# Kernel optimization log

Hardware: AMD Instinct MI355X
Metric: run time of the kernel (lower is better)

The kernel has to match this reference:

```python
import jax, jax.numpy as jnp
import numpy as np

B, S, H, D = 4, 1024, 16, 64
DM = H * D  # 1024
SCALE = float(np.sqrt(D))


def setup_inputs() -> dict:
    key = jax.random.key(0)
    ks = jax.random.split(key, 7)
    mk = lambda k, shp: jax.random.normal(k, shp, dtype=jnp.float32)
    return {
        "query": mk(ks[0], (B, S, DM)),
        "key": mk(ks[1], (B, S, DM)),
        "value": mk(ks[2], (B, S, DM)),
        "Wq": mk(ks[3], (DM, DM)) * 0.02,
        "Wk": mk(ks[4], (DM, DM)) * 0.02,
        "Wv": mk(ks[5], (DM, DM)) * 0.02,
        "Wo": mk(ks[6], (DM, DM)) * 0.02,
    }


def reference(query, key, value, Wq, Wk, Wv, Wo):
    b, s, _ = query.shape
    # nn.Linear(x) = x @ W.T ; reshape to (b, h, s, d)
    Q = (query @ Wq.T).reshape(b, s, H, D).transpose(0, 2, 1, 3)
    K = (key @ Wk.T).reshape(b, s, H, D).transpose(0, 2, 1, 3)
    V = (value @ Wv.T).reshape(b, s, H, D).transpose(0, 2, 1, 3)
    scores = jnp.einsum("bhqd,bhkd->bhqk", Q, K) / SCALE
    attn = jax.nn.softmax(scores, axis=-1)  # dropout p=0 -> identity
    ctx = jnp.einsum("bhqk,bhkd->bhqd", attn, V)
    ctx = ctx.transpose(0, 2, 1, 3).reshape(b, s, DM)
    out = ctx @ Wo.T
    return out, attn
```

## Files before the change

kernel.cpp:

```cpp
#include <hip/hip_runtime.h>
#include <hip/hip_bf16.h>
#include <stdint.h>


#define DEV static __device__ __forceinline__

typedef __bf16 bf16x8 __attribute__((ext_vector_type(8)));
typedef float f32x4 __attribute__((ext_vector_type(4)));
typedef unsigned short u16x8 __attribute__((ext_vector_type(8)));

static constexpr int B = 4, S = 1024, H = 16, D = 64, DM = 1024;
static constexpr int M = B * S;

DEV uint16_t f2bf_bits(float f) {
    __hip_bfloat16 h = __float2bfloat16(f);
    return __builtin_bit_cast(uint16_t, h);
}
DEV uint64_t pack4(float4 v) {
    return (uint64_t)f2bf_bits(v.x) | ((uint64_t)f2bf_bits(v.y) << 16) |
           ((uint64_t)f2bf_bits(v.z) << 32) | ((uint64_t)f2bf_bits(v.w) << 48);
}
DEV bf16x8 ldfrag(const uint16_t* p) {
    u16x8 t = *(const u16x8*)p;
    return __builtin_bit_cast(bf16x8, t);
}

#define GLOAD16(g, l)                                                  \
    __builtin_amdgcn_global_load_lds(                                  \
        (const __attribute__((address_space(1))) void*)(g),            \
        (__attribute__((address_space(3))) void*)(l), 16, 0, 0)

#define MFMA16(a, b, c) __builtin_amdgcn_mfma_f32_16x16x32_bf16(a, b, c, 0, 0, 0)

__global__ __launch_bounds__(256) void cvt_w4(const float* __restrict__ w0,
                                              const float* __restrict__ w1,
                                              const float* __restrict__ w2,
                                              const float* __restrict__ w3,
                                              uint16_t* __restrict__ dst) {
    const float* srcs[4] = {w0, w1, w2, w3};
    const float* src = srcs[blockIdx.y];
    uint16_t* d = dst + (size_t)blockIdx.y * DM * DM;
    int i = (blockIdx.x * 256 + threadIdx.x) * 8;
    float4 a = *(const float4*)(src + i);
    float4 b = *(const float4*)(src + i + 4);
    *(uint64_t*)(d + i) = pack4(a);
    *(uint64_t*)(d + i + 4) = pack4(b);
}

__global__ __launch_bounds__(256) void gemm_qkv(const float* __restrict__ qa,
                                                const float* __restrict__ ka,
                                                const float* __restrict__ va,
                                                const uint16_t* __restrict__ Wb,
                                                uint16_t* __restrict__ Qb,
                                                uint16_t* __restrict__ Kb,
                                                uint16_t* __restrict__ Vt) {
    constexpr int BK = 32;
    __shared__ uint16_t Ah[128 * BK];
    __shared__ uint16_t Bh[128 * BK];
    const int tid = threadIdx.x;
    const int lane = tid & 63, wid = tid >> 6;
    const int lr = lane & 15, lg = lane >> 4;
    const int m0 = blockIdx.x * 128, n0 = blockIdx.y * 128;
    const int z = blockIdx.z;
    const int wr = (wid >> 1) * 64, wc = (wid & 1) * 64;

    const float* A = z == 0 ? qa : (z == 1 ? ka : va);
    const uint16_t* W = Wb + (size_t)z * DM * DM;
    uint16_t* Cp = z == 0 ? Qb : (z == 1 ? Kb : Vt);

    const int arow = tid >> 1, acs = (tid & 1) * 16;
    const int brow = wid * 16 + (lane >> 2), bcol = (lane & 3) * 8;

    f32x4 acc[4][4] = {};

    for (int kb = 0; kb < DM / BK; ++kb) {
        const float* ap = A + (size_t)(m0 + arow) * DM + kb * BK + acs;
        float4 v0 = *(const float4*)(ap + 0);
        float4 v1 = *(const float4*)(ap + 4);
        float4 v2 = *(const float4*)(ap + 8);
        float4 v3 = *(const float4*)(ap + 12);
#pragma unroll
        for (int c = 0; c < 2; ++c) {
            int row = c * 64 + brow;
            GLOAD16(W + (size_t)(n0 + row) * DM + kb * BK + bcol, Bh + row * BK + bcol);
        }
        uint16_t* aw = Ah + arow * BK + acs;
        *(uint64_t*)(aw + 0) = pack4(v0);
        *(uint64_t*)(aw + 4) = pack4(v1);
        *(uint64_t*)(aw + 8) = pack4(v2);
        *(uint64_t*)(aw + 12) = pack4(v3);
        __syncthreads();

        bf16x8 af[4], bw[4];
#pragma unroll
        for (int i = 0; i < 4; ++i) af[i] = ldfrag(&Ah[(wr + i * 16 + lr) * BK + lg * 8]);
#pragma unroll
        for (int i = 0; i < 4; ++i) bw[i] = ldfrag(&Bh[(wc + i * 16 + lr) * BK + lg * 8]);
#pragma unroll
        for (int mi = 0; mi < 4; ++mi)
#pragma unroll
            for (int ni = 0; ni < 4; ++ni)
                acc[mi][ni] = MFMA16(af[mi], bw[ni], acc[mi][ni]);
        __syncthreads();
    }

#pragma unroll
    for (int mi = 0; mi < 4; ++mi)
#pragma unroll
        for (int ni = 0; ni < 4; ++ni)
#pragma unroll
            for (int r = 0; r < 4; ++r) {
                int gm = m0 + wr + mi * 16 + lg * 4 + r;
                int gn = n0 + wc + ni * 16 + lr;
                uint16_t v = f2bf_bits(acc[mi][ni][r]);
                int b = gm >> 10, s = gm & 1023, h = gn >> 6, d = gn & 63;
                if (z != 2)
                    Cp[((size_t)(b * H + h) * S + s) * D + d] = v;
                else
                    Cp[((size_t)(b * H + h) * D + d) * S + s] = v;
            }
}

__global__ __launch_bounds__(256) void gemm_o(const uint16_t* __restrict__ ctx,
                                              const uint16_t* __restrict__ Wo,
                                              float* __restrict__ out) {
    constexpr int BK = 32;
    __shared__ uint16_t Ah[128 * BK];
    __shared__ uint16_t Bh[128 * BK];
    const int tid = threadIdx.x;
    const int lane = tid & 63, wid = tid >> 6;
    const int lr = lane & 15, lg = lane >> 4;
    const int m0 = blockIdx.x * 128, n0 = blockIdx.y * 128;
    const int wr = (wid >> 1) * 64, wc = (wid & 1) * 64;
    const int srow = wid * 16 + (lane >> 2), scol = (lane & 3) * 8;

    f32x4 acc[4][4] = {};

    for (int kb = 0; kb < DM / BK; ++kb) {
#pragma unroll
        for (int c = 0; c < 2; ++c) {
            int row = c * 64 + srow;
            GLOAD16(ctx + (size_t)(m0 + row) * DM + kb * BK + scol, Ah + row * BK + scol);
            GLOAD16(Wo + (size_t)(n0 + row) * DM + kb * BK + scol, Bh + row * BK + scol);
        }
        __syncthreads();

        bf16x8 af[4], bw[4];
#pragma unroll
        for (int i = 0; i < 4; ++i) af[i] = ldfrag(&Ah[(wr + i * 16 + lr) * BK + lg * 8]);
#pragma unroll
        for (int i = 0; i < 4; ++i) bw[i] = ldfrag(&Bh[(wc + i * 16 + lr) * BK + lg * 8]);
#pragma unroll
        for (int mi = 0; mi < 4; ++mi)
#pragma unroll
            for (int ni = 0; ni < 4; ++ni)
                acc[mi][ni] = MFMA16(af[mi], bw[ni], acc[mi][ni]);
        __syncthreads();
    }

#pragma unroll
    for (int mi = 0; mi < 4; ++mi)
#pragma unroll
        for (int ni = 0; ni < 4; ++ni)
#pragma unroll
            for (int r = 0; r < 4; ++r) {
                int gm = m0 + wr + mi * 16 + lg * 4 + r;
                int gn = n0 + wc + ni * 16 + lr;
                out[(size_t)gm * DM + gn] = acc[mi][ni][r];
            }
}

__global__ __launch_bounds__(256) void attn_fused(const uint16_t* __restrict__ Qb,
                                                  const uint16_t* __restrict__ Kb,
                                                  const uint16_t* __restrict__ Vt,
                                                  float* __restrict__ attn,
                                                  uint16_t* __restrict__ ctx) {
    __shared__ uint16_t plds[4][16][40];
    const int tid = threadIdx.x, lane = tid & 63, wid = tid >> 6;
    const int lr = lane & 15, lg = lane >> 4;
    const int wg = blockIdx.x;
    const int xcd = wg & 7, rr_ = wg >> 3;
    const int qt = rr_ & 15, bh = xcd + 8 * (rr_ >> 4);
    const int q0 = qt * 64 + wid * 16;

    const uint16_t* Qp = Qb + ((size_t)bh * S + q0) * D;
    const bf16x8 aq0 = ldfrag(Qp + lr * D + lg * 8);
    const bf16x8 aq1 = ldfrag(Qp + lr * D + 32 + lg * 8);

    const uint16_t* Kbase = Kb + (size_t)bh * S * D;
    constexpr float CEXP = 0.125f * 1.44269504088896340736f;

    float lsum[4] = {0.f, 0.f, 0.f, 0.f};
    for (int kc = 0; kc < S / 32; ++kc) {
        const uint16_t* Kp = Kbase + (size_t)kc * 32 * D;
        bf16x8 k00 = ldfrag(Kp + lr * D + lg * 8);
        bf16x8 k01 = ldfrag(Kp + lr * D + 32 + lg * 8);
        bf16x8 k10 = ldfrag(Kp + (16 + lr) * D + lg * 8);
        bf16x8 k11 = ldfrag(Kp + (16 + lr) * D + 32 + lg * 8);
        f32x4 s0 = {}, s1 = {};
        s0 = MFMA16(aq0, k00, s0);
        s0 = MFMA16(aq1, k01, s0);
        s1 = MFMA16(aq0, k10, s1);
        s1 = MFMA16(aq1, k11, s1);
#pragma unroll
        for (int r = 0; r < 4; ++r)
            lsum[r] += exp2f(s0[r] * CEXP) + exp2f(s1[r] * CEXP);
    }
#pragma unroll
    for (int r = 0; r < 4; ++r) {
        float v = lsum[r];
        v += __shfl_xor(v, 1);
        v += __shfl_xor(v, 2);
        v += __shfl_xor(v, 4);
        v += __shfl_xor(v, 8);
        lsum[r] = 1.0f / v;
    }

    f32x4 cacc[4] = {};
    float* attn_base = attn + (size_t)bh * S * S + (size_t)q0 * S;
    const uint16_t* Vbase = Vt + (size_t)bh * D * S;
    uint16_t(*pw)[40] = plds[wid];

    for (int kc = 0; kc < S / 32; ++kc) {
        const uint16_t* Kp = Kbase + (size_t)kc * 32 * D;
        bf16x8 k00 = ldfrag(Kp + lr * D + lg * 8);
        bf16x8 k01 = ldfrag(Kp + lr * D + 32 + lg * 8);
        bf16x8 k10 = ldfrag(Kp + (16 + lr) * D + lg * 8);
        bf16x8 k11 = ldfrag(Kp + (16 + lr) * D + 32 + lg * 8);
        bf16x8 bv[4];
#pragma unroll
        for (int dt = 0; dt < 4; ++dt)
            bv[dt] = ldfrag(Vbase + (size_t)(dt * 16 + lr) * S + kc * 32 + lg * 8);
        f32x4 s0 = {}, s1 = {};
        s0 = MFMA16(aq0, k00, s0);
        s0 = MFMA16(aq1, k01, s0);
        s1 = MFMA16(aq0, k10, s1);
        s1 = MFMA16(aq1, k11, s1);
#pragma unroll
        for (int r = 0; r < 4; ++r) {
            float p0 = exp2f(s0[r] * CEXP) * lsum[r];
            float p1 = exp2f(s1[r] * CEXP) * lsum[r];
            attn_base[(size_t)(lg * 4 + r) * S + kc * 32 + lr] = p0;
            attn_base[(size_t)(lg * 4 + r) * S + kc * 32 + 16 + lr] = p1;
            pw[lg * 4 + r][lr] = f2bf_bits(p0);
            pw[lg * 4 + r][16 + lr] = f2bf_bits(p1);
        }
        asm volatile("s_waitcnt lgkmcnt(0)" ::: "memory");
        bf16x8 pa = ldfrag(&pw[lr][lg * 8]);
#pragma unroll
        for (int dt = 0; dt < 4; ++dt)
            cacc[dt] = MFMA16(pa, bv[dt], cacc[dt]);
    }

    const int b = bh >> 4, h = bh & 15;
#pragma unroll
    for (int dt = 0; dt < 4; ++dt)
#pragma unroll
        for (int r = 0; r < 4; ++r) {
            int q = q0 + lg * 4 + r;
            int d = dt * 16 + lr;
            ctx[((size_t)b * S + q) * DM + h * D + d] = f2bf_bits(cacc[dt][r]);
        }
}

extern "C" void kernel_launch(void* const* d_in, const int* in_sizes, int n_in,
                              void* d_out, int out_size, void* d_ws, size_t ws_size,
                              hipStream_t stream) {
    const float* q = (const float*)d_in[0];
    const float* k = (const float*)d_in[1];
    const float* v = (const float*)d_in[2];
    const float* Wq = (const float*)d_in[3];
    const float* Wk = (const float*)d_in[4];
    const float* Wv = (const float*)d_in[5];
    const float* Wo = (const float*)d_in[6];

    float* out = (float*)d_out;
    float* attn = out + (size_t)B * S * DM;

    const size_t NQ = (size_t)B * H * S * D;
    uint16_t* Qb = (uint16_t*)d_ws;
    uint16_t* Kb = Qb + NQ;
    uint16_t* Vt = Kb + NQ;
    uint16_t* ctx = Vt + NQ;
    uint16_t* Wb = ctx + NQ;

    cvt_w4<<<dim3(512, 4), 256, 0, stream>>>(Wq, Wk, Wv, Wo, Wb);
    gemm_qkv<<<dim3(M / 128, DM / 128, 3), 256, 0, stream>>>(q, k, v, Wb, Qb, Kb, Vt);
    attn_fused<<<dim3(16 * 64), 256, 0, stream>>>(Qb, Kb, Vt, attn, ctx);
    gemm_o<<<dim3(M / 128, DM / 128), 256, 0, stream>>>(ctx, Wb + (size_t)3 * DM * DM, out);
}
```

Measured before the change: 561.9 us.

## Stage K/V in LDS with swizzle, coalesce attn stores, widen GEMM K tiles

The attention kernel now double-buffers K and V tiles in swizzled LDS through async global-to-LDS loads. Probabilities are staged in LDS as fp32 so the attn matrix is written with coalesced float4 stores. Both GEMMs move to BK=64, and the V projection transposes through LDS so Vt is written with vector stores. When the workspace is large enough, the activations are pre-converted to bf16 in a single conversion kernel so the QKV GEMM loads them asynchronously. The trade is extra LDS use and block-wide barriers in the attention loop.

```diff
diff --git a/kernel.cpp b/kernel.cpp
--- a/kernel.cpp
+++ b/kernel.cpp
@@ -9,8 +9,8 @@
 typedef float f32x4 __attribute__((ext_vector_type(4)));
 typedef unsigned short u16x8 __attribute__((ext_vector_type(8)));
 
-static constexpr int B = 4, S = 1024, H = 16, D = 64, DM = 1024;
-static constexpr int M = B * S;
+static constexpr int B = 4, S = 1024, H = 16, D = 64, DM = 1024, M = 4096;
+static constexpr size_t NQ = (size_t)M * DM;
 
 DEV uint16_t f2bf_bits(float f) {
     __hip_bfloat16 h = __float2bfloat16(f);
@@ -19,6 +19,10 @@
 DEV uint64_t pack4(float4 v) {
     return (uint64_t)f2bf_bits(v.x) | ((uint64_t)f2bf_bits(v.y) << 16) |
            ((uint64_t)f2bf_bits(v.z) << 32) | ((uint64_t)f2bf_bits(v.w) << 48);
+}
+DEV uint64_t pack4f(const f32x4& v) {
+    return (uint64_t)f2bf_bits(v[0]) | ((uint64_t)f2bf_bits(v[1]) << 16) |
+           ((uint64_t)f2bf_bits(v[2]) << 32) | ((uint64_t)f2bf_bits(v[3]) << 48);
 }
 DEV bf16x8 ldfrag(const uint16_t* p) {
     u16x8 t = *(const u16x8*)p;
@@ -31,6 +35,27 @@
         (__attribute__((address_space(3))) void*)(l), 16, 0, 0)
 
 #define MFMA16(a, b, c) __builtin_amdgcn_mfma_f32_16x16x32_bf16(a, b, c, 0, 0, 0)
+
+__global__ __launch_bounds__(256) void cvt_all(const float* __restrict__ q,
+                                               const float* __restrict__ k,
+                                               const float* __restrict__ v,
+                                               const float* __restrict__ wq,
+                                               const float* __restrict__ wk,
+                                               const float* __restrict__ wv,
+                                               const float* __restrict__ wo,
+                                               uint16_t* __restrict__ dst) {
+    const int y = blockIdx.y;
+    const float* srcs[7] = {q, k, v, wq, wk, wv, wo};
+    const float* src = srcs[y];
+    const size_t base = y < 3 ? (size_t)y * NQ : 3 * NQ + (size_t)(y - 3) * (DM * DM);
+    const size_t n = y < 3 ? NQ : (size_t)DM * DM;
+    size_t i = ((size_t)blockIdx.x * 256 + threadIdx.x) * 8;
+    if (i >= n) return;
+    float4 a = *(const float4*)(src + i);
+    float4 b2 = *(const float4*)(src + i + 4);
+    *(uint64_t*)(dst + base + i) = pack4(a);
+    *(uint64_t*)(dst + base + i + 4) = pack4(b2);
+}
 
 __global__ __launch_bounds__(256) void cvt_w4(const float* __restrict__ w0,
                                               const float* __restrict__ w1,
@@ -42,119 +67,149 @@
     uint16_t* d = dst + (size_t)blockIdx.y * DM * DM;
     int i = (blockIdx.x * 256 + threadIdx.x) * 8;
     float4 a = *(const float4*)(src + i);
-    float4 b = *(const float4*)(src + i + 4);
+    float4 b2 = *(const float4*)(src + i + 4);
     *(uint64_t*)(d + i) = pack4(a);
-    *(uint64_t*)(d + i + 4) = pack4(b);
-}
-
+    *(uint64_t*)(d + i + 4) = pack4(b2);
+}
+
+template <int AF32>
 __global__ __launch_bounds__(256) void gemm_qkv(const float* __restrict__ qa,
                                                 const float* __restrict__ ka,
                                                 const float* __restrict__ va,
+                                                const uint16_t* __restrict__ xb,
                                                 const uint16_t* __restrict__ Wb,
                                                 uint16_t* __restrict__ Qb,
                                                 uint16_t* __restrict__ Kb,
                                                 uint16_t* __restrict__ Vt) {
-    constexpr int BK = 32;
-    __shared__ uint16_t Ah[128 * BK];
-    __shared__ uint16_t Bh[128 * BK];
-    const int tid = threadIdx.x;
-    const int lane = tid & 63, wid = tid >> 6;
+    constexpr int BK = 64, ALD = AF32 ? 72 : 64;
+    __shared__ __align__(16) uint16_t smem[17408];
+    uint16_t* Ah = smem;
+    uint16_t* Bh = smem + (AF32 ? 9216 : 8192);
+    const int tid = threadIdx.x, lane = tid & 63, wid = tid >> 6;
     const int lr = lane & 15, lg = lane >> 4;
-    const int m0 = blockIdx.x * 128, n0 = blockIdx.y * 128;
-    const int z = blockIdx.z;
+    const int m0 = blockIdx.x * 128, n0 = blockIdx.y * 128, z = blockIdx.z;
     const int wr = (wid >> 1) * 64, wc = (wid & 1) * 64;
 
-    const float* A = z == 0 ? qa : (z == 1 ? ka : va);
-    const uint16_t* W = Wb + (size_t)z * DM * DM;
-    uint16_t* Cp = z == 0 ? Qb : (z == 1 ? Kb : Vt);
-
-    const int arow = tid >> 1, acs = (tid & 1) * 16;
-    const int brow = wid * 16 + (lane >> 2), bcol = (lane & 3) * 8;
+    const float* Af = z == 0 ? qa : (z == 1 ? ka : va);
+    const uint16_t* Ab = xb + (size_t)z * NQ;
+    const uint16_t* W = Wb + (size_t)z * (DM * DM);
 
     f32x4 acc[4][4] = {};
 
     for (int kb = 0; kb < DM / BK; ++kb) {
-        const float* ap = A + (size_t)(m0 + arow) * DM + kb * BK + acs;
-        float4 v0 = *(const float4*)(ap + 0);
-        float4 v1 = *(const float4*)(ap + 4);
-        float4 v2 = *(const float4*)(ap + 8);
-        float4 v3 = *(const float4*)(ap + 12);
-#pragma unroll
-        for (int c = 0; c < 2; ++c) {
-            int row = c * 64 + brow;
-            GLOAD16(W + (size_t)(n0 + row) * DM + kb * BK + bcol, Bh + row * BK + bcol);
-        }
-        uint16_t* aw = Ah + arow * BK + acs;
-        *(uint64_t*)(aw + 0) = pack4(v0);
-        *(uint64_t*)(aw + 4) = pack4(v1);
-        *(uint64_t*)(aw + 8) = pack4(v2);
-        *(uint64_t*)(aw + 12) = pack4(v3);
-        __syncthreads();
-
-        bf16x8 af[4], bw[4];
-#pragma unroll
-        for (int i = 0; i < 4; ++i) af[i] = ldfrag(&Ah[(wr + i * 16 + lr) * BK + lg * 8]);
-#pragma unroll
-        for (int i = 0; i < 4; ++i) bw[i] = ldfrag(&Bh[(wc + i * 16 + lr) * BK + lg * 8]);
+        if constexpr (AF32) {
+#pragma unroll
+            for (int i = 0; i < 8; ++i) {
+                int f = tid + i * 256;
+                int row = f >> 4, c4 = (f & 15) * 4;
+                float4 vv = *(const float4*)(Af + (size_t)(m0 + row) * DM + kb * BK + c4);
+                *(uint64_t*)&Ah[row * ALD + c4] = pack4(vv);
+            }
+        } else {
+#pragma unroll
+            for (int p = 0; p < 4; ++p) {
+                int row = p * 32 + (tid >> 3), ce = (tid & 7) * 8;
+                GLOAD16(Ab + (size_t)(m0 + row) * DM + kb * BK + ce, Ah + row * 64 + ce);
+            }
+        }
+#pragma unroll
+        for (int p = 0; p < 4; ++p) {
+            int row = p * 32 + (tid >> 3), ce = (tid & 7) * 8;
+            GLOAD16(W + (size_t)(n0 + row) * DM + kb * BK + ce, Bh + row * 64 + ce);
+        }
+        __syncthreads();
+
+        bf16x8 af[4][2], bw[4][2];
+#pragma unroll
+        for (int i = 0; i < 4; ++i)
+#pragma unroll
+            for (int ks = 0; ks < 2; ++ks) {
+                af[i][ks] = ldfrag(&Ah[(wr + i * 16 + lr) * ALD + ks * 32 + lg * 8]);
+                bw[i][ks] = ldfrag(&Bh[(wc + i * 16 + lr) * 64 + ks * 32 + lg * 8]);
+            }
+#pragma unroll
+        for (int ks = 0; ks < 2; ++ks)
+#pragma unroll
+            for (int mi = 0; mi < 4; ++mi)
+#pragma unroll
+                for (int ni = 0; ni < 4; ++ni)
+                    acc[mi][ni] = MFMA16(af[mi][ks], bw[ni][ks], acc[mi][ni]);
+        __syncthreads();
+    }
+
+    if (z != 2) {
+        uint16_t* Cp = z == 0 ? Qb : Kb;
 #pragma unroll
         for (int mi = 0; mi < 4; ++mi)
 #pragma unroll
             for (int ni = 0; ni < 4; ++ni)
-                acc[mi][ni] = MFMA16(af[mi], bw[ni], acc[mi][ni]);
-        __syncthreads();
-    }
-
-#pragma unroll
-    for (int mi = 0; mi < 4; ++mi)
-#pragma unroll
-        for (int ni = 0; ni < 4; ++ni)
-#pragma unroll
-            for (int r = 0; r < 4; ++r) {
-                int gm = m0 + wr + mi * 16 + lg * 4 + r;
-                int gn = n0 + wc + ni * 16 + lr;
-                uint16_t v = f2bf_bits(acc[mi][ni][r]);
-                int b = gm >> 10, s = gm & 1023, h = gn >> 6, d = gn & 63;
-                if (z != 2)
-                    Cp[((size_t)(b * H + h) * S + s) * D + d] = v;
-                else
-                    Cp[((size_t)(b * H + h) * D + d) * S + s] = v;
-            }
+#pragma unroll
+                for (int r = 0; r < 4; ++r) {
+                    int gm = m0 + wr + mi * 16 + lg * 4 + r;
+                    int gn = n0 + wc + ni * 16 + lr;
+                    int b = gm >> 10, s = gm & 1023, h = gn >> 6, d = gn & 63;
+                    Cp[((size_t)(b * H + h) * S + s) * D + d] = f2bf_bits(acc[mi][ni][r]);
+                }
+    } else {
+        uint16_t* T = smem;
+#pragma unroll
+        for (int mi = 0; mi < 4; ++mi)
+#pragma unroll
+            for (int ni = 0; ni < 4; ++ni) {
+                int row = wc + ni * 16 + lr;
+                int colb = wr + mi * 16 + lg * 4;
+                *(uint64_t*)&T[row * 136 + colb] = pack4f(acc[mi][ni]);
+            }
+        __syncthreads();
+        const int b = m0 >> 10, s0b = m0 & 1023;
+#pragma unroll
+        for (int p = 0; p < 8; ++p) {
+            int row = p * 16 + (tid >> 4), sl = tid & 15;
+            int h = (n0 + row) >> 6, d = (n0 + row) & 63;
+            u16x8 val = *(u16x8*)&T[row * 136 + sl * 8];
+            *(u16x8*)&Vt[((size_t)(b * H + h) * D + d) * S + s0b + sl * 8] = val;
+        }
+    }
 }
 
 __global__ __launch_bounds__(256) void gemm_o(const uint16_t* __restrict__ ctx,
                                               const uint16_t* __restrict__ Wo,
                                               float* __restrict__ out) {
-    constexpr int BK = 32;
-    __shared__ uint16_t Ah[128 * BK];
-    __shared__ uint16_t Bh[128 * BK];
-    const int tid = threadIdx.x;
-    const int lane = tid & 63, wid = tid >> 6;
+    constexpr int BK = 64;
+    __shared__ __align__(16) uint16_t smem[16384];
+    uint16_t* Ah = smem;
+    uint16_t* Bh = smem + 8192;
+    const int tid = threadIdx.x, lane = tid & 63, wid = tid >> 6;
     const int lr = lane & 15, lg = lane >> 4;
     const int m0 = blockIdx.x * 128, n0 = blockIdx.y * 128;
     const int wr = (wid >> 1) * 64, wc = (wid & 1) * 64;
-    const int srow = wid * 16 + (lane >> 2), scol = (lane & 3) * 8;
 
     f32x4 acc[4][4] = {};
 
     for (int kb = 0; kb < DM / BK; ++kb) {
 #pragma unroll
-        for (int c = 0; c < 2; ++c) {
-            int row = c * 64 + srow;
-            GLOAD16(ctx + (size_t)(m0 + row) * DM + kb * BK + scol, Ah + row * BK + scol);
-            GLOAD16(Wo + (size_t)(n0 + row) * DM + kb * BK + scol, Bh + row * BK + scol);
-        }
-        __syncthreads();
-
-        bf16x8 af[4], bw[4];
-#pragma unroll
-        for (int i = 0; i < 4; ++i) af[i] = ldfrag(&Ah[(wr + i * 16 + lr) * BK + lg * 8]);
-#pragma unroll
-        for (int i = 0; i < 4; ++i) bw[i] = ldfrag(&Bh[(wc + i * 16 + lr) * BK + lg * 8]);
-#pragma unroll
-        for (int mi = 0; mi < 4; ++mi)
-#pragma unroll
-            for (int ni = 0; ni < 4; ++ni)
-                acc[mi][ni] = MFMA16(af[mi], bw[ni], acc[mi][ni]);
+        for (int p = 0; p < 4; ++p) {
+            int row = p * 32 + (tid >> 3), ce = (tid & 7) * 8;
+            GLOAD16(ctx + (size_t)(m0 + row) * DM + kb * BK + ce, Ah + row * 64 + ce);
+            GLOAD16(Wo + (size_t)(n0 + row) * DM + kb * BK + ce, Bh + row * 64 + ce);
+        }
+        __syncthreads();
+
+        bf16x8 af[4][2], bw[4][2];
+#pragma unroll
+        for (int i = 0; i < 4; ++i)
+#pragma unroll
+            for (int ks = 0; ks < 2; ++ks) {
+                af[i][ks] = ldfrag(&Ah[(wr + i * 16 + lr) * 64 + ks * 32 + lg * 8]);
+                bw[i][ks] = ldfrag(&Bh[(wc + i * 16 + lr) * 64 + ks * 32 + lg * 8]);
+            }
+#pragma unroll
+        for (int ks = 0; ks < 2; ++ks)
+#pragma unroll
+            for (int mi = 0; mi < 4; ++mi)
+#pragma unroll
+                for (int ni = 0; ni < 4; ++ni)
+                    acc[mi][ni] = MFMA16(af[mi][ks], bw[ni][ks], acc[mi][ni]);
         __syncthreads();
     }
 
@@ -175,7 +230,9 @@
                                                   const uint16_t* __restrict__ Vt,
                                                   float* __restrict__ attn,
                                                   uint16_t* __restrict__ ctx) {
-    __shared__ uint16_t plds[4][16][40];
+    __shared__ __align__(16) uint16_t Kl[2][2048];
+    __shared__ __align__(16) uint16_t Vl[2][2048];
+    __shared__ __align__(16) float pf[4][16 * 36];
     const int tid = threadIdx.x, lane = tid & 63, wid = tid >> 6;
     const int lr = lane & 15, lg = lane >> 4;
     const int wg = blockIdx.x;
@@ -188,15 +245,25 @@
     const bf16x8 aq1 = ldfrag(Qp + lr * D + 32 + lg * 8);
 
     const uint16_t* Kbase = Kb + (size_t)bh * S * D;
+    const uint16_t* Vbase = Vt + (size_t)bh * D * S;
     constexpr float CEXP = 0.125f * 1.44269504088896340736f;
 
+    const int krow = tid >> 3, kslot = (tid & 7) ^ ((tid >> 3) & 7);
+    const int vrow = tid >> 2, vslot = (tid & 3) ^ ((tid >> 3) & 3);
+
+#define STAGE_K(buf, kc) GLOAD16(Kbase + (size_t)((kc)*32 + krow) * D + kslot * 8, &Kl[buf][tid * 8])
+#define STAGE_V(buf, kc) GLOAD16(Vbase + (size_t)vrow * S + (kc)*32 + vslot * 8, &Vl[buf][tid * 8])
+#define KFRAG(buf, t, h) ldfrag(&Kl[buf][((t)*16 + lr) * 64 + ((((h)*4 + lg) ^ (lr & 7)) * 8)])
+#define VFRAG(buf, dt) ldfrag(&Vl[buf][((dt)*16 + lr) * 32 + ((lg ^ ((lr >> 1) & 3)) * 8)])
+
     float lsum[4] = {0.f, 0.f, 0.f, 0.f};
+    STAGE_K(0, 0);
+    __syncthreads();
     for (int kc = 0; kc < S / 32; ++kc) {
-        const uint16_t* Kp = Kbase + (size_t)kc * 32 * D;
-        bf16x8 k00 = ldfrag(Kp + lr * D + lg * 8);
-        bf16x8 k01 = ldfrag(Kp + lr * D + 32 + lg * 8);
-        bf16x8 k10 = ldfrag(Kp + (16 + lr) * D + lg * 8);
-        bf16x8 k11 = ldfrag(Kp + (16 + lr) * D + 32 + lg * 8);
+        const int buf = kc & 1;
+        if (kc < S / 32 - 1) STAGE_K(buf ^ 1, kc + 1);
+        bf16x8 k00 = KFRAG(buf, 0, 0), k01 = KFRAG(buf, 0, 1);
+        bf16x8 k10 = KFRAG(buf, 1, 0), k11 = KFRAG(buf, 1, 1);
         f32x4 s0 = {}, s1 = {};
         s0 = MFMA16(aq0, k00, s0);
         s0 = MFMA16(aq1, k01, s0);
@@ -205,6 +272,7 @@
 #pragma unroll
         for (int r = 0; r < 4; ++r)
             lsum[r] += exp2f(s0[r] * CEXP) + exp2f(s1[r] * CEXP);
+        __syncthreads();
     }
 #pragma unroll
     for (int r = 0; r < 4; ++r) {
@@ -218,19 +286,19 @@
 
     f32x4 cacc[4] = {};
     float* attn_base = attn + (size_t)bh * S * S + (size_t)q0 * S;
-    const uint16_t* Vbase = Vt + (size_t)bh * D * S;
-    uint16_t(*pw)[40] = plds[wid];
-
+    float* pfw = pf[wid];
+
+    STAGE_K(0, 0);
+    STAGE_V(0, 0);
+    __syncthreads();
     for (int kc = 0; kc < S / 32; ++kc) {
-        const uint16_t* Kp = Kbase + (size_t)kc * 32 * D;
-        bf16x8 k00 = ldfrag(Kp + lr * D + lg * 8);
-        bf16x8 k01 = ldfrag(Kp + lr * D + 32 + lg * 8);
-        bf16x8 k10 = ldfrag(Kp + (16 + lr) * D + lg * 8);
-        bf16x8 k11 = ldfrag(Kp + (16 + lr) * D + 32 + lg * 8);
-        bf16x8 bv[4];
-#pragma unroll
-        for (int dt = 0; dt < 4; ++dt)
-            bv[dt] = ldfrag(Vbase + (size_t)(dt * 16 + lr) * S + kc * 32 + lg * 8);
+        const int buf = kc & 1;
+        if (kc < S / 32 - 1) {
+            STAGE_K(buf ^ 1, kc + 1);
+            STAGE_V(buf ^ 1, kc + 1);
+        }
+        bf16x8 k00 = KFRAG(buf, 0, 0), k01 = KFRAG(buf, 0, 1);
+        bf16x8 k10 = KFRAG(buf, 1, 0), k11 = KFRAG(buf, 1, 1);
         f32x4 s0 = {}, s1 = {};
         s0 = MFMA16(aq0, k00, s0);
         s0 = MFMA16(aq1, k01, s0);
@@ -238,18 +306,36 @@
         s1 = MFMA16(aq1, k11, s1);
 #pragma unroll
         for (int r = 0; r < 4; ++r) {
-            float p0 = exp2f(s0[r] * CEXP) * lsum[r];
-            float p1 = exp2f(s1[r] * CEXP) * lsum[r];
-            attn_base[(size_t)(lg * 4 + r) * S + kc * 32 + lr] = p0;
-            attn_base[(size_t)(lg * 4 + r) * S + kc * 32 + 16 + lr] = p1;
-            pw[lg * 4 + r][lr] = f2bf_bits(p0);
-            pw[lg * 4 + r][16 + lr] = f2bf_bits(p1);
+            pfw[(lg * 4 + r) * 36 + lr] = exp2f(s0[r] * CEXP) * lsum[r];
+            pfw[(lg * 4 + r) * 36 + 16 + lr] = exp2f(s1[r] * CEXP) * lsum[r];
         }
         asm volatile("s_waitcnt lgkmcnt(0)" ::: "memory");
-        bf16x8 pa = ldfrag(&pw[lr][lg * 8]);
-#pragma unroll
-        for (int dt = 0; dt < 4; ++dt)
-            cacc[dt] = MFMA16(pa, bv[dt], cacc[dt]);
+        {
+            const float* rp = &pfw[(lane >> 2) * 36 + (lane & 3) * 4];
+            float4 a0 = *(const float4*)rp;
+            float4 a1 = *(const float4*)(rp + 16);
+            float* gp = attn_base + (size_t)(lane >> 2) * S + kc * 32 + (lane & 3) * 4;
+            *(float4*)gp = a0;
+            *(float4*)(gp + 16) = a1;
+        }
+        bf16x8 pa;
+        {
+            const f32x4 p0 = *(const f32x4*)&pfw[lr * 36 + lg * 8];
+            const f32x4 p1 = *(const f32x4*)&pfw[lr * 36 + lg * 8 + 4];
+            u16x8 pu;
+#pragma unroll
+            for (int j = 0; j < 4; ++j) {
+                pu[j] = f2bf_bits(p0[j]);
+                pu[4 + j] = f2bf_bits(p1[j]);
+            }
+            pa = __builtin_bit_cast(bf16x8, pu);
+        }
+#pragma unroll
+        for (int dt = 0; dt < 4; ++dt) {
+            bf16x8 bv = VFRAG(buf, dt);
+            cacc[dt] = MFMA16(pa, bv, cacc[dt]);
+        }
+        __syncthreads();
     }
 
     const int b = bh >> 4, h = bh & 15;
@@ -261,6 +347,10 @@
             int d = dt * 16 + lr;
             ctx[((size_t)b * S + q) * DM + h * D + d] = f2bf_bits(cacc[dt][r]);
         }
+#undef STAGE_K
+#undef STAGE_V
+#undef KFRAG
+#undef VFRAG
 }
 
 extern "C" void kernel_launch(void* const* d_in, const int* in_sizes, int n_in,
@@ -277,15 +367,29 @@
     float* out = (float*)d_out;
     float* attn = out + (size_t)B * S * DM;
 
-    const size_t NQ = (size_t)B * H * S * D;
-    uint16_t* Qb = (uint16_t*)d_ws;
-    uint16_t* Kb = Qb + NQ;
-    uint16_t* Vt = Kb + NQ;
-    uint16_t* ctx = Vt + NQ;
-    uint16_t* Wb = ctx + NQ;
-
-    cvt_w4<<<dim3(512, 4), 256, 0, stream>>>(Wq, Wk, Wv, Wo, Wb);
-    gemm_qkv<<<dim3(M / 128, DM / 128, 3), 256, 0, stream>>>(q, k, v, Wb, Qb, Kb, Vt);
-    attn_fused<<<dim3(16 * 64), 256, 0, stream>>>(Qb, Kb, Vt, attn, ctx);
-    gemm_o<<<dim3(M / 128, DM / 128), 256, 0, stream>>>(ctx, Wb + (size_t)3 * DM * DM, out);
-}
+    const bool big = ws_size >= (size_t)7 * NQ * 2 + 256;
+    dim3 gg(M / 128, DM / 128, 3);
+
+    if (big) {
+        uint16_t* xb = (uint16_t*)d_ws;
+        uint16_t* Wb = xb + 3 * NQ;
+        uint16_t* Qb = Wb + NQ;
+        uint16_t* Kb = Qb + NQ;
+        uint16_t* Vt = Kb + NQ;
+        uint16_t* ctx = xb;
+        cvt_all<<<dim3(2048, 7), 256, 0, stream>>>(q, k, v, Wq, Wk, Wv, Wo, xb);
+        gemm_qkv<0><<<gg, 256, 0, stream>>>(q, k, v, xb, Wb, Qb, Kb, Vt);
+        attn_fused<<<dim3(1024), 256, 0, stream>>>(Qb, Kb, Vt, attn, ctx);
+        gemm_o<<<dim3(M / 128, DM / 128), 256, 0, stream>>>(ctx, Wb + (size_t)3 * DM * DM, out);
+    } else {
+        uint16_t* Qb = (uint16_t*)d_ws;
+        uint16_t* Kb = Qb + NQ;
+        uint16_t* Vt = Kb + NQ;
+        uint16_t* ctx = Vt + NQ;
+        uint16_t* Wb = ctx + NQ;
+        cvt_w4<<<dim3(512, 4), 256, 0, stream>>>(Wq, Wk, Wv, Wo, Wb);
+        gemm_qkv<1><<<gg, 256, 0, stream>>>(q, k, v, nullptr, Wb, Qb, Kb, Vt);
+        attn_fused<<<dim3(1024), 256, 0, stream>>>(Qb, Kb, Vt, attn, ctx);
+        gemm_o<<<dim3(M / 128, DM / 128), 256, 0, stream>>>(ctx, Wb + (size_t)3 * DM * DM, out);
+    }
+}
```

New measurement: 456.9 us. 18.7% less time.
